# Performance work log

Measured on AMD Instinct MI355X. Metric: run time of the kernel, lower is better.

## Reference

```python
import jax, jax.numpy as jnp
import numpy as np

N_NODES = 50000
N_EDGES = 500000
NEG_SLOPE = 0.2


def gat_conv(h, src, dst, W, attn_l, attn_r, bias, activation):
    """DGL-style GATConv (feat_drop=attn_drop=0, no residual).
    h: [N, F_in]; W: [F_in, H*D]; attn_l/attn_r: [H, D]; bias: [H*D].
    Returns [N, H, D]."""
    H, D = attn_l.shape
    feat = (h @ W).reshape(-1, H, D)                      # [N, H, D]
    el = (feat * attn_l).sum(-1)                          # [N, H]
    er = (feat * attn_r).sum(-1)                          # [N, H]
    e = jax.nn.leaky_relu(el[src] + er[dst], NEG_SLOPE)   # [E, H] edge logits
    # edge softmax over incoming edges of each dst node
    emax = jax.ops.segment_max(e, dst, num_segments=N_NODES)
    emax = jnp.where(jnp.isfinite(emax), emax, 0.0)       # guard zero in-degree
    ee = jnp.exp(e - emax[dst])                           # [E, H]
    denom = jax.ops.segment_sum(ee, dst, num_segments=N_NODES)
    alpha = ee / jnp.maximum(denom[dst], 1e-9)            # [E, H]
    # weighted scatter-aggregate of source features
    out = jax.ops.segment_sum(feat[src] * alpha[..., None], dst,
                              num_segments=N_NODES)       # [N, H, D]
    out = out + bias.reshape(1, H, D)
    return activation(out) if activation is not None else out


def setup_inputs() -> dict:
    key = jax.random.key(0)
    ks = jax.random.split(key, 20)
    in0, in1, hid, heads, ncls = 256, 128, 64, 8, 10

    def xn(k, shape):
        fan = shape[0] + (shape[1] if len(shape) > 1 else shape[0])
        return jax.random.normal(k, shape, jnp.float32) * np.float32(np.sqrt(2.0 / fan)) * 1.414

    inp = {
        "feat0": jax.random.normal(ks[0], (30000, in0), jnp.float32),
        "feat1": jax.random.normal(ks[1], (20000, in1), jnp.float32),
        "fc0_w": xn(ks[2], (in0, hid)), "fc0_b": jnp.zeros((hid,), jnp.float32),
        "fc1_w": xn(ks[3], (in1, hid)), "fc1_b": jnp.zeros((hid,), jnp.float32),
        "W0": xn(ks[4], (hid, heads * hid)),
        "al0": xn(ks[5], (heads, hid)), "ar0": xn(ks[6], (heads, hid)),
        "b0": jnp.zeros((heads * hid,), jnp.float32),
        "W1": xn(ks[7], (heads * hid, heads * hid)),
        "al1": xn(ks[8], (heads, hid)), "ar1": xn(ks[9], (heads, hid)),
        "b1": jnp.zeros((heads * hid,), jnp.float32),
        "W2": xn(ks[10], (heads * hid, 1 * ncls)),
        "al2": xn(ks[11], (1, ncls)), "ar2": xn(ks[12], (1, ncls)),
        "b2": jnp.zeros((ncls,), jnp.float32),
        "edge_index": jax.random.randint(ks[13], (2, N_EDGES), 0, N_NODES, jnp.int64
                                         if jax.config.jax_enable_x64 else jnp.int32),
    }
    return inp


def reference(feat0, feat1, fc0_w, fc0_b, fc1_w, fc1_b,
              W0, al0, ar0, b0, W1, al1, ar1, b1, W2, al2, ar2, b2,
              edge_index):
    src, dst = edge_index[0], edge_index[1]
    # per-type linear projection then concat along node axis
    h = jnp.concatenate([feat0 @ fc0_w + fc0_b, feat1 @ fc1_w + fc1_b], axis=0)
    h = gat_conv(h, src, dst, W0, al0, ar0, b0, jax.nn.elu).reshape(N_NODES, -1)
    h = gat_conv(h, src, dst, W1, al1, ar1, b1, jax.nn.elu).reshape(N_NODES, -1)
    logits = gat_conv(h, src, dst, W2, al2, ar2, b2, None).mean(axis=1)  # [N, ncls]
    return logits
```

## Files before the change

### kernel.cpp

```cpp
#include <hip/hip_runtime.h>
#include <hip/hip_bf16.h>
#include <hip/hip_fp16.h>

#define N_NODES 50000
#define N_EDGES 500000
#define HEADS 8
#define HID 64
#define HD 512
#define NCLS 10
#define M_PAD 50048
#define YTILES_L1 391
#define F0ROWS 30080
#define F1ROWS 20096

typedef _Float16 f16x8 __attribute__((ext_vector_type(8)));
typedef _Float16 h8v   __attribute__((ext_vector_type(8)));
typedef float    f32x4 __attribute__((ext_vector_type(4)));

#define GLD_LDS16(g, l) __builtin_amdgcn_global_load_lds( \
    (__attribute__((address_space(1))) void*)(g),         \
    (__attribute__((address_space(3))) void*)(l), 16, 0, 0)

#define E_N (F0ROWS * 256)
#define F_N (F1ROWS * 128)
#define A_N (512 * 256)
#define B_N (512 * 128)
#define C_N (512 * 512)
#define D_N 1024
#define PREP_TOTAL (E_N + F_N + A_N + B_N + C_N + D_N + N_EDGES)

__global__ void prep(const float* __restrict__ feat0, const float* __restrict__ feat1,
                     const float* __restrict__ fc0_w, const float* __restrict__ fc0_b,
                     const float* __restrict__ fc1_w, const float* __restrict__ fc1_b,
                     const float* __restrict__ W0, const float* __restrict__ W1,
                     const int* __restrict__ dst,
                     _Float16* __restrict__ f0h, _Float16* __restrict__ f1h,
                     _Float16* __restrict__ Wc0t, _Float16* __restrict__ Wc1t,
                     _Float16* __restrict__ W1t, float* __restrict__ biasF,
                     int* __restrict__ cnt) {
    int idx = blockIdx.x * 256 + threadIdx.x;
    if (idx < E_N) {
        int m = idx >> 8, k = idx & 255;
        f0h[idx] = (m < 30000) ? (_Float16)feat0[(size_t)m * 256 + k] : (_Float16)0.f;
        return;
    }
    idx -= E_N;
    if (idx < F_N) {
        int m = idx >> 7, k = idx & 127;
        f1h[idx] = (m < 20000) ? (_Float16)feat1[(size_t)m * 128 + k] : (_Float16)0.f;
        return;
    }
    idx -= F_N;
    if (idx < A_N) {
        int k = idx >> 9, n = idx & 511;
        float s = 0.f;
#pragma unroll 8
        for (int j = 0; j < 64; j++) s += fc0_w[k * 64 + j] * W0[j * 512 + n];
        Wc0t[n * 256 + k] = (_Float16)s;
        return;
    }
    idx -= A_N;
    if (idx < B_N) {
        int k = idx >> 9, n = idx & 511;
        float s = 0.f;
#pragma unroll 8
        for (int j = 0; j < 64; j++) s += fc1_w[k * 64 + j] * W0[j * 512 + n];
        Wc1t[n * 128 + k] = (_Float16)s;
        return;
    }
    idx -= B_N;
    if (idx < C_N) {
        int k = idx >> 9, n = idx & 511;
        W1t[n * 512 + k] = (_Float16)W1[k * 512 + n];
        return;
    }
    idx -= C_N;
    if (idx < D_N) {
        int t = idx >> 9, n = idx & 511;
        const float* fb = t ? fc1_b : fc0_b;
        float s = 0.f;
#pragma unroll 8
        for (int j = 0; j < 64; j++) s += fb[j] * W0[j * 512 + n];
        biasF[t * 512 + n] = s;
        return;
    }
    idx -= D_N;
    if (idx < N_EDGES) atomicAdd(&cnt[dst[idx]], 1);
}

#define NBLK_SCAN 196

__global__ void scan_part(const int* __restrict__ cnt, int* __restrict__ part) {
    __shared__ int s[256];
    int i = blockIdx.x * 256 + threadIdx.x;
    s[threadIdx.x] = (i < N_NODES) ? cnt[i] : 0;
    __syncthreads();
    for (int off = 128; off; off >>= 1) {
        if (threadIdx.x < off) s[threadIdx.x] += s[threadIdx.x + off];
        __syncthreads();
    }
    if (threadIdx.x == 0) part[blockIdx.x] = s[0];
}

__global__ void scan_offs(int* __restrict__ part) {
    __shared__ int s[256];
    int tid = threadIdx.x;
    int v = (tid < NBLK_SCAN) ? part[tid] : 0;
    s[tid] = v;
    __syncthreads();
    for (int off = 1; off < 256; off <<= 1) {
        int x = (tid >= off) ? s[tid - off] : 0;
        __syncthreads();
        s[tid] += x;
        __syncthreads();
    }
    if (tid < NBLK_SCAN) part[tid] = s[tid] - v;
}

__global__ void scan_apply(const int* __restrict__ cnt, const int* __restrict__ part,
                           int* __restrict__ rp, int* __restrict__ cur) {
    __shared__ int s[256];
    int tid = threadIdx.x;
    int i = blockIdx.x * 256 + tid;
    int v = (i < N_NODES) ? cnt[i] : 0;
    s[tid] = v;
    __syncthreads();
    for (int off = 1; off < 256; off <<= 1) {
        int x = (tid >= off) ? s[tid - off] : 0;
        __syncthreads();
        s[tid] += x;
        __syncthreads();
    }
    if (i < N_NODES) {
        int excl = s[tid] - v + part[blockIdx.x];
        rp[i] = excl; cur[i] = excl;
    }
    if (i == 0) rp[N_NODES] = N_EDGES;
}

__device__ __forceinline__ void gemm_tile(
        const _Float16* __restrict__ A, const _Float16* __restrict__ Bt,
        _Float16* __restrict__ Cb, const float* __restrict__ al,
        const float* __restrict__ ar, const float* __restrict__ cbias,
        float* __restrict__ el, float* __restrict__ er,
        int M, int K, int row_off, int ytiles, int bid,
        _Float16* Asl, _Float16* Bsl) {
    int k8 = bid & 7, jj = bid >> 3;
    int y = k8 + 8 * (jj >> 1);
    if (y >= ytiles) return;
    int m0 = y * 128;
    int n0 = (jj & 1) * 256;
    int t = threadIdx.x;
    int lane = t & 63;
    int w = t >> 6;
    int wm = (w & 1) * 64, wn = (w >> 1) * 64;
    int l15 = lane & 15, quad = lane >> 4;
    f32x4 acc[4][4];
#pragma unroll
    for (int i = 0; i < 4; i++)
#pragma unroll
        for (int j = 0; j < 4; j++) acc[i][j] = (f32x4){0.f, 0.f, 0.f, 0.f};

    int fbA = t * 16;
    int rowA = fbA >> 6, kgA = ((fbA >> 4) & 3) ^ (rowA & 3);
    int fbB0 = t * 16;
    int fbB1 = fbB0 + 8192;
    int rowB0 = fbB0 >> 6, kgB0 = ((fbB0 >> 4) & 3) ^ (rowB0 & 3);
    int rowB1 = fbB1 >> 6, kgB1 = ((fbB1 >> 4) & 3) ^ (rowB1 & 3);

    for (int k0 = 0; k0 < K; k0 += 32) {
        GLD_LDS16(A + (size_t)(m0 + rowA) * K + k0 + kgA * 8, (char*)Asl + fbA);
        GLD_LDS16(Bt + (size_t)(n0 + rowB0) * K + k0 + kgB0 * 8, (char*)Bsl + fbB0);
        GLD_LDS16(Bt + (size_t)(n0 + rowB1) * K + k0 + kgB1 * 8, (char*)Bsl + fbB1);
        __syncthreads();
        f16x8 af[4], bfr[4];
#pragma unroll
        for (int i = 0; i < 4; i++) {
            int r = wm + i * 16 + l15;
            int kg = quad ^ (r & 3);
            af[i] = *(const f16x8*)(Asl + r * 32 + kg * 8);
        }
#pragma unroll
        for (int j = 0; j < 4; j++) {
            int r = wn + j * 16 + l15;
            int kg = quad ^ (r & 3);
            bfr[j] = *(const f16x8*)(Bsl + r * 32 + kg * 8);
        }
#pragma unroll
        for (int i = 0; i < 4; i++)
#pragma unroll
            for (int j = 0; j < 4; j++)
                acc[i][j] = __builtin_amdgcn_mfma_f32_16x16x32_f16(af[i], bfr[j], acc[i][j], 0, 0, 0);
        __syncthreads();
    }
    float cb[4];
#pragma unroll
    for (int j = 0; j < 4; j++)
        cb[j] = cbias ? cbias[n0 + wn + j * 16 + l15] : 0.f;
#pragma unroll
    for (int i = 0; i < 4; i++) {
        int rbase = m0 + wm + i * 16 + quad * 4;
#pragma unroll
        for (int j = 0; j < 4; j++) {
            int col = n0 + wn + j * 16 + l15;
#pragma unroll
            for (int r = 0; r < 4; r++) {
                int row = rbase + r;
                if (row < M)
                    Cb[(size_t)(row_off + row) * HD + col] = (_Float16)(acc[i][j][r] + cb[j]);
            }
        }
    }
    int h = (n0 + wn) >> 6;
    float alv[4], arv[4];
#pragma unroll
    for (int j = 0; j < 4; j++) {
        alv[j] = al[h * 64 + j * 16 + l15];
        arv[j] = ar[h * 64 + j * 16 + l15];
    }
#pragma unroll
    for (int i = 0; i < 4; i++) {
#pragma unroll
        for (int r = 0; r < 4; r++) {
            float sl = 0.f, sr = 0.f;
#pragma unroll
            for (int j = 0; j < 4; j++) {
                float v = acc[i][j][r] + cb[j];
                sl += v * alv[j]; sr += v * arv[j];
            }
#pragma unroll
            for (int mk = 1; mk < 16; mk <<= 1) {
                sl += __shfl_xor(sl, mk);
                sr += __shfl_xor(sr, mk);
            }
            int row = m0 + wm + i * 16 + quad * 4 + r;
            if (l15 == 0 && row < M) {
                el[(size_t)(row_off + row) * HEADS + h] = sl;
                er[(size_t)(row_off + row) * HEADS + h] = sr;
            }
        }
    }
}

#define SCAT_BLKS ((N_EDGES + 511) / 512)
#define G0A_BLKS (8 * 2 * ((235 + 7) / 8))
#define G0B_BLKS (8 * 2 * ((157 + 7) / 8))

__global__ __launch_bounds__(512) void scatter_gemm0(
        const int* __restrict__ src, const int* __restrict__ dst,
        int* __restrict__ cursor, int* __restrict__ srcs,
        const _Float16* __restrict__ f0h, const _Float16* __restrict__ Wc0t,
        const _Float16* __restrict__ f1h, const _Float16* __restrict__ Wc1t,
        _Float16* __restrict__ featA, const float* __restrict__ al0,
        const float* __restrict__ ar0, const float* __restrict__ biasF,
        float* __restrict__ el, float* __restrict__ er) {
    __shared__ _Float16 Asl[128 * 32];
    __shared__ _Float16 Bsl[256 * 32];
    int bid = blockIdx.x;
    if (bid < SCAT_BLKS) {
        int t = bid * 512 + threadIdx.x;
        if (t < N_EDGES) {
            int pos = atomicAdd(&cursor[dst[t]], 1);
            srcs[pos] = src[t];
        }
        return;
    }
    bid -= SCAT_BLKS;
    if (bid < G0A_BLKS) {
        gemm_tile(f0h, Wc0t, featA, al0, ar0, biasF, el, er,
                  30000, 256, 0, 235, bid, Asl, Bsl);
        return;
    }
    bid -= G0A_BLKS;
    gemm_tile(f1h, Wc1t, featA, al0, ar0, biasF + 512, el, er,
              20000, 128, 30000, 157, bid, Asl, Bsl);
}

__global__ __launch_bounds__(512) void gemm_mfma_wide(const _Float16* __restrict__ A,
                                                      const _Float16* __restrict__ Bt,
                                                      _Float16* __restrict__ Cb,
                                                      const float* __restrict__ al,
                                                      const float* __restrict__ ar,
                                                      float* __restrict__ el,
                                                      float* __restrict__ er,
                                                      int M, int K, int ytiles) {
    __shared__ _Float16 Asl[128 * 32];
    __shared__ _Float16 Bsl[256 * 32];
    gemm_tile(A, Bt, Cb, al, ar, nullptr, el, er, M, K, 0, ytiles,
              blockIdx.x, Asl, Bsl);
}

__global__ __launch_bounds__(64) void attn_agg(
        const int* __restrict__ rp, const int* __restrict__ srcs,
        const float* __restrict__ el, const float* __restrict__ er,
        const _Float16* __restrict__ feat, const float* __restrict__ bias,
        _Float16* __restrict__ out) {
    __shared__ float aS[592];
    __shared__ int   sS[64];
    int lane = threadIdx.x;
    int n    = blockIdx.x;
    int s0 = rp[n], s1 = rp[n + 1];
    int deg = s1 - s0;
    float er8[8];
    {
        f32x4 a = *(const f32x4*)(er + (size_t)n * 8);
        f32x4 b = *(const f32x4*)(er + (size_t)n * 8 + 4);
        er8[0]=a[0]; er8[1]=a[1]; er8[2]=a[2]; er8[3]=a[3];
        er8[4]=b[0]; er8[5]=b[1]; er8[6]=b[2]; er8[7]=b[3];
    }
    bool fast = (deg <= 64);
    if (fast) {
        bool act = lane < deg;
        int sp = act ? srcs[s0 + lane] : 0;
        sS[lane] = sp;
        f32x4 ea = {0.f,0.f,0.f,0.f}, eb = {0.f,0.f,0.f,0.f};
        if (act) {
            ea = *(const f32x4*)(el + (size_t)sp * 8);
            eb = *(const f32x4*)(el + (size_t)sp * 8 + 4);
        }
        float e8[8] = {ea[0],ea[1],ea[2],ea[3],eb[0],eb[1],eb[2],eb[3]};
#pragma unroll
        for (int h = 0; h < 8; h++) {
            float e = e8[h] + er8[h];
            e = e > 0.f ? e : 0.2f * e;
            e8[h] = act ? e : -1e30f;
        }
#pragma unroll
        for (int h = 0; h < 8; h++) {
            float mm = e8[h];
#pragma unroll
            for (int mk = 1; mk < 64; mk <<= 1) mm = fmaxf(mm, __shfl_xor(mm, mk));
            float pv = act ? __expf(e8[h] - mm) : 0.f;
            float ss = pv;
#pragma unroll
            for (int mk = 1; mk < 64; mk <<= 1) ss += __shfl_xor(ss, mk);
            aS[lane * 9 + h] = pv * (1.f / fmaxf(ss, 1e-9f));
        }
    } else {
        float m8[8], s8[8];
#pragma unroll
        for (int h = 0; h < 8; h++) { m8[h] = -1e30f; s8[h] = 0.f; }
        for (int base = s0; base < s1; base += 64) {
            bool act = base + lane < s1;
            int sp = act ? srcs[base + lane] : 0;
            f32x4 ea = {0.f,0.f,0.f,0.f}, eb = {0.f,0.f,0.f,0.f};
            if (act) {
                ea = *(const f32x4*)(el + (size_t)sp * 8);
                eb = *(const f32x4*)(el + (size_t)sp * 8 + 4);
            }
            float ev[8] = {ea[0],ea[1],ea[2],ea[3],eb[0],eb[1],eb[2],eb[3]};
#pragma unroll
            for (int h = 0; h < 8; h++) {
                float e = ev[h] + er8[h];
                e = e > 0.f ? e : 0.2f * e;
                e = act ? e : -1e30f;
                float cm = e;
#pragma unroll
                for (int mk = 1; mk < 64; mk <<= 1) cm = fmaxf(cm, __shfl_xor(cm, mk));
                float nm = fmaxf(m8[h], cm);
                float pv = act ? __expf(e - nm) : 0.f;
#pragma unroll
                for (int mk = 1; mk < 64; mk <<= 1) pv += __shfl_xor(pv, mk);
                s8[h] = s8[h] * __expf(m8[h] - nm) + pv;
                m8[h] = nm;
            }
        }
        if (lane == 0) {
#pragma unroll
            for (int h = 0; h < 8; h++) {
                aS[576 + h] = 1.f / fmaxf(s8[h], 1e-9f);
                aS[584 + h] = m8[h];
            }
        }
    }
    __builtin_amdgcn_wave_barrier();
    int hh = lane >> 3, d0 = (lane & 7) * 8;
    h8v z = {(_Float16)0, (_Float16)0, (_Float16)0, (_Float16)0,
             (_Float16)0, (_Float16)0, (_Float16)0, (_Float16)0};
    h8v acc0 = z, acc1 = z, acc2 = z, acc3 = z;
    const _Float16* colbase = feat + hh * 64 + d0;
    if (fast) {
        int p = 0;
        for (; p + 4 <= deg; p += 4) {
            int spa = sS[p],     spb = sS[p + 1];
            int spc = sS[p + 2], spd = sS[p + 3];
            _Float16 aa = (_Float16)aS[p * 9 + hh];
            _Float16 ab = (_Float16)aS[(p + 1) * 9 + hh];
            _Float16 ac = (_Float16)aS[(p + 2) * 9 + hh];
            _Float16 ad = (_Float16)aS[(p + 3) * 9 + hh];
            h8v fa = *(const h8v*)(colbase + (size_t)spa * HD);
            h8v fb = *(const h8v*)(colbase + (size_t)spb * HD);
            h8v fc = *(const h8v*)(colbase + (size_t)spc * HD);
            h8v fd = *(const h8v*)(colbase + (size_t)spd * HD);
            h8v a8a = {aa, aa, aa, aa, aa, aa, aa, aa};
            h8v a8b = {ab, ab, ab, ab, ab, ab, ab, ab};
            h8v a8c = {ac, ac, ac, ac, ac, ac, ac, ac};
            h8v a8d = {ad, ad, ad, ad, ad, ad, ad, ad};
            acc0 += a8a * fa;
            acc1 += a8b * fb;
            acc2 += a8c * fc;
            acc3 += a8d * fd;
        }
        for (; p < deg; p++) {
            int sp = sS[p];
            _Float16 ah = (_Float16)aS[p * 9 + hh];
            h8v a8 = {ah, ah, ah, ah, ah, ah, ah, ah};
            h8v f = *(const h8v*)(colbase + (size_t)sp * HD);
            acc0 += a8 * f;
        }
    } else {
        float inv_l = aS[576 + hh];
        float m_l   = aS[584 + hh];
        float ern_l = er[(size_t)n * 8 + hh];
        for (int p = s0; p < s1; p++) {
            int sp = srcs[p];
            float e = el[(size_t)sp * 8 + hh] + ern_l;
            e = e > 0.f ? e : 0.2f * e;
            _Float16 ah = (_Float16)(__expf(e - m_l) * inv_l);
            h8v a8 = {ah, ah, ah, ah, ah, ah, ah, ah};
            h8v f = *(const h8v*)(colbase + (size_t)sp * HD);
            acc0 += a8 * f;
        }
    }
    acc0 += acc1; acc2 += acc3; acc0 += acc2;
    float4 b0v = *(const float4*)(bias + lane * 8);
    float4 b1v = *(const float4*)(bias + lane * 8 + 4);
    float bb[8] = {b0v.x,b0v.y,b0v.z,b0v.w,b1v.x,b1v.y,b1v.z,b1v.w};
    h8v o;
#pragma unroll
    for (int j = 0; j < 8; j++) {
        float x = (float)acc0[j] + bb[j];
        x = x > 0.f ? x : __expf(x) - 1.f;
        o[j] = (_Float16)x;
    }
    *(h8v*)(out + (size_t)n * HD + lane * 8) = o;
}

__global__ __launch_bounds__(256) void gemm_n10v2(
        const _Float16* __restrict__ A, const float* __restrict__ B,
        const float* __restrict__ al2, const float* __restrict__ ar2,
        float* __restrict__ C, float* __restrict__ el, float* __restrict__ er) {
    __shared__ float Bs[512 * 11];
    int t = threadIdx.x;
    for (int i = t; i < 512 * NCLS; i += 256) {
        int k = i / NCLS, c = i - k * NCLS;
        Bs[k * 11 + c] = B[i];
    }
    __syncthreads();
    int lane = t & 63;
    int m = blockIdx.x * 4 + (t >> 6);
    float acc[NCLS];
#pragma unroll
    for (int c = 0; c < NCLS; c++) acc[c] = 0.f;
    const _Float16* a = A + (size_t)m * HD;
#pragma unroll
    for (int j = 0; j < 8; j++) {
        float av = (float)a[j * 64 + lane];
        const float* br = Bs + (j * 64 + lane) * 11;
#pragma unroll
        for (int c = 0; c < NCLS; c++) acc[c] += av * br[c];
    }
#pragma unroll
    for (int c = 0; c < NCLS; c++)
#pragma unroll
        for (int mk = 1; mk < 64; mk <<= 1) acc[c] += __shfl_xor(acc[c], mk);
    if (lane == 0) {
        float e1 = 0.f, e2 = 0.f;
#pragma unroll
        for (int c = 0; c < NCLS; c++) { e1 += acc[c] * al2[c]; e2 += acc[c] * ar2[c]; }
        el[m] = e1; er[m] = e2;
#pragma unroll
        for (int c = 0; c < NCLS; c++) C[(size_t)m * NCLS + c] = acc[c];
    }
}

__global__ __launch_bounds__(64) void attn2_agg2(
        const int* __restrict__ rp, const int* __restrict__ srcs,
        const float* __restrict__ el, const float* __restrict__ er,
        const float* __restrict__ feat2, const float* __restrict__ b2,
        float* __restrict__ out) {
    int lane = threadIdx.x;
    int n = blockIdx.x;
    int s0 = rp[n], s1 = rp[n + 1], deg = s1 - s0;
    float ern = er[n];
    float facc[NCLS];
#pragma unroll
    for (int c = 0; c < NCLS; c++) facc[c] = 0.f;
    if (deg <= 64) {
        bool act = lane < deg;
        int sp = act ? srcs[s0 + lane] : 0;
        float e = act ? el[sp] + ern : 0.f;
        e = e > 0.f ? e : 0.2f * e;
        if (!act) e = -1e30f;
        float mm = e;
#pragma unroll
        for (int mk = 1; mk < 64; mk <<= 1) mm = fmaxf(mm, __shfl_xor(mm, mk));
        float pv = act ? __expf(e - mm) : 0.f;
        float ss = pv;
#pragma unroll
        for (int mk = 1; mk < 64; mk <<= 1) ss += __shfl_xor(ss, mk);
        float a = pv / fmaxf(ss, 1e-9f);
        if (act) {
#pragma unroll
            for (int c = 0; c < NCLS; c++) facc[c] = a * feat2[(size_t)sp * NCLS + c];
        }
    } else {
        float mm = -1e30f, ssum = 0.f;
        for (int base = s0; base < s1; base += 64) {
            bool act = base + lane < s1;
            int sp = act ? srcs[base + lane] : 0;
            float e = act ? el[sp] + ern : 0.f;
            e = e > 0.f ? e : 0.2f * e;
            if (!act) e = -1e30f;
            float cm = e;
#pragma unroll
            for (int mk = 1; mk < 64; mk <<= 1) cm = fmaxf(cm, __shfl_xor(cm, mk));
            float nm = fmaxf(mm, cm);
            float pv = act ? __expf(e - nm) : 0.f;
#pragma unroll
            for (int mk = 1; mk < 64; mk <<= 1) pv += __shfl_xor(pv, mk);
            ssum = ssum * __expf(mm - nm) + pv;
            mm = nm;
        }
        float inv = 1.f / fmaxf(ssum, 1e-9f);
        for (int base = s0; base < s1; base += 64) {
            bool act = base + lane < s1;
            int sp = act ? srcs[base + lane] : 0;
            float e = act ? el[sp] + ern : 0.f;
            e = e > 0.f ? e : 0.2f * e;
            float a = act ? __expf(e - mm) * inv : 0.f;
            if (act) {
#pragma unroll
                for (int c = 0; c < NCLS; c++) facc[c] += a * feat2[(size_t)sp * NCLS + c];
            }
        }
    }
#pragma unroll
    for (int c = 0; c < NCLS; c++)
#pragma unroll
        for (int mk = 1; mk < 64; mk <<= 1) facc[c] += __shfl_xor(facc[c], mk);
    if (lane == 0) {
#pragma unroll
        for (int c = 0; c < NCLS; c++) out[(size_t)n * NCLS + c] = facc[c] + b2[c];
    }
}

extern "C" void kernel_launch(void* const* d_in, const int* in_sizes, int n_in,
                              void* d_out, int out_size, void* d_ws, size_t ws_size,
                              hipStream_t stream) {
    const float* feat0 = (const float*)d_in[0];
    const float* feat1 = (const float*)d_in[1];
    const float* fc0_w = (const float*)d_in[2];
    const float* fc0_b = (const float*)d_in[3];
    const float* fc1_w = (const float*)d_in[4];
    const float* fc1_b = (const float*)d_in[5];
    const float* W0    = (const float*)d_in[6];
    const float* al0   = (const float*)d_in[7];
    const float* ar0   = (const float*)d_in[8];
    const float* b0    = (const float*)d_in[9];
    const float* W1    = (const float*)d_in[10];
    const float* al1   = (const float*)d_in[11];
    const float* ar1   = (const float*)d_in[12];
    const float* b1    = (const float*)d_in[13];
    const float* W2    = (const float*)d_in[14];
    const float* al2   = (const float*)d_in[15];
    const float* ar2   = (const float*)d_in[16];
    const float* b2    = (const float*)d_in[17];
    const int* eidx    = (const int*)d_in[18];
    const int* src = eidx;
    const int* dst = eidx + N_EDGES;
    float* out = (float*)d_out;

    char* ws = (char*)d_ws;
    size_t off = 0;
    auto alloc = [&](size_t bytes) { size_t o = off; off = (off + bytes + 255) & ~(size_t)255; return o; };

    _Float16* featA = (_Float16*)(ws + alloc((size_t)M_PAD * HD * 2));
    _Float16* aggh  = (_Float16*)(ws + alloc((size_t)M_PAD * HD * 2));
    _Float16* f0h   = (_Float16*)(ws + alloc((size_t)F0ROWS * 256 * 2));
    _Float16* f1h   = (_Float16*)(ws + alloc((size_t)F1ROWS * 128 * 2));
    float*    feat2 = (float*)(ws + alloc((size_t)N_NODES * NCLS * 4));
    float*    el    = (float*)(ws + alloc((size_t)N_NODES * HEADS * 4));
    float*    er    = (float*)(ws + alloc((size_t)N_NODES * HEADS * 4));
    float*    el2   = (float*)(ws + alloc((size_t)N_NODES * 4));
    float*    er2   = (float*)(ws + alloc((size_t)N_NODES * 4));
    float*    biasF = (float*)(ws + alloc(1024 * 4));
    int*      cnt   = (int*)  (ws + alloc((size_t)N_NODES * 4));
    int*      rp    = (int*)  (ws + alloc((size_t)(N_NODES + 1) * 4));
    int*      cur   = (int*)  (ws + alloc((size_t)N_NODES * 4));
    int*      srcs  = (int*)  (ws + alloc((size_t)N_EDGES * 4));
    int*      part  = (int*)  (ws + alloc(1024));
    _Float16* Wc0t  = (_Float16*)(ws + alloc(512 * 256 * 2));
    _Float16* Wc1t  = (_Float16*)(ws + alloc(512 * 128 * 2));
    _Float16* W1t   = (_Float16*)(ws + alloc(512 * 512 * 2));

    hipMemsetAsync(cnt, 0, N_NODES * sizeof(int), stream);
    prep<<<(PREP_TOTAL + 255) / 256, 256, 0, stream>>>(
        feat0, feat1, fc0_w, fc0_b, fc1_w, fc1_b, W0, W1, dst,
        f0h, f1h, Wc0t, Wc1t, W1t, biasF, cnt);

    scan_part<<<NBLK_SCAN, 256, 0, stream>>>(cnt, part);
    scan_offs<<<1, 256, 0, stream>>>(part);
    scan_apply<<<NBLK_SCAN, 256, 0, stream>>>(cnt, part, rp, cur);

    scatter_gemm0<<<SCAT_BLKS + G0A_BLKS + G0B_BLKS, 512, 0, stream>>>(
        src, dst, cur, srcs, f0h, Wc0t, f1h, Wc1t, featA, al0, ar0, biasF, el, er);

    attn_agg<<<N_NODES, 64, 0, stream>>>(rp, srcs, el, er, featA, b0, aggh);

    int g1 = 8 * 2 * ((YTILES_L1 + 7) / 8);
    gemm_mfma_wide<<<g1, 512, 0, stream>>>(aggh, W1t, featA, al1, ar1, el, er,
                                           N_NODES, HD, YTILES_L1);
    attn_agg<<<N_NODES, 64, 0, stream>>>(rp, srcs, el, er, featA, b1, aggh);

    gemm_n10v2<<<N_NODES / 4, 256, 0, stream>>>(aggh, W2, al2, ar2, feat2, el2, er2);
    attn2_agg2<<<N_NODES, 64, 0, stream>>>(rp, srcs, el2, er2, feat2, b2, out);
}
```

Measured before the change: 529.5 us.

## Pack four destination nodes per wave in attention aggregation kernel

Reworks the attention-aggregate kernel so each 64-lane wave handles four destination nodes with 16 lanes each, rather than one node per wave. Each lane now covers 32 output columns across four head pairs, and the softmax reductions use 16-lane shuffles. The aim is to cut wasted lanes and per-block overhead, since average in-degree is about 10 and most lanes sat idle before. In exchange, nodes with degree above 16 take the slower online-softmax path, and the four nodes in a wave can diverge on degree.

```diff
diff --git a/kernel.cpp b/kernel.cpp
--- a/kernel.cpp
+++ b/kernel.cpp
@@ -290,15 +290,18 @@
               blockIdx.x, Asl, Bsl);
 }
 
-__global__ __launch_bounds__(64) void attn_agg(
+__global__ __launch_bounds__(64) void attn_agg4(
         const int* __restrict__ rp, const int* __restrict__ srcs,
         const float* __restrict__ el, const float* __restrict__ er,
         const _Float16* __restrict__ feat, const float* __restrict__ bias,
         _Float16* __restrict__ out) {
-    __shared__ float aS[592];
+    __shared__ float aS[576];
     __shared__ int   sS[64];
     int lane = threadIdx.x;
-    int n    = blockIdx.x;
+    int g    = lane >> 4;
+    int gl   = lane & 15;
+    int hi   = gl >> 3;
+    int n    = blockIdx.x * 4 + g;
     int s0 = rp[n], s1 = rp[n + 1];
     int deg = s1 - s0;
     float er8[8];
@@ -308,10 +311,11 @@
         er8[0]=a[0]; er8[1]=a[1]; er8[2]=a[2]; er8[3]=a[3];
         er8[4]=b[0]; er8[5]=b[1]; er8[6]=b[2]; er8[7]=b[3];
     }
-    bool fast = (deg <= 64);
+    bool fast = (deg <= 16);
+    float m8[8], s8[8];
     if (fast) {
-        bool act = lane < deg;
-        int sp = act ? srcs[s0 + lane] : 0;
+        bool act = gl < deg;
+        int sp = act ? srcs[s0 + gl] : 0;
         sS[lane] = sp;
         f32x4 ea = {0.f,0.f,0.f,0.f}, eb = {0.f,0.f,0.f,0.f};
         if (act) {
@@ -329,20 +333,19 @@
         for (int h = 0; h < 8; h++) {
             float mm = e8[h];
 #pragma unroll
-            for (int mk = 1; mk < 64; mk <<= 1) mm = fmaxf(mm, __shfl_xor(mm, mk));
+            for (int mk = 1; mk < 16; mk <<= 1) mm = fmaxf(mm, __shfl_xor(mm, mk));
             float pv = act ? __expf(e8[h] - mm) : 0.f;
             float ss = pv;
 #pragma unroll
-            for (int mk = 1; mk < 64; mk <<= 1) ss += __shfl_xor(ss, mk);
-            aS[lane * 9 + h] = pv * (1.f / fmaxf(ss, 1e-9f));
+            for (int mk = 1; mk < 16; mk <<= 1) ss += __shfl_xor(ss, mk);
+            aS[g * 144 + gl * 9 + h] = pv * (1.f / fmaxf(ss, 1e-9f));
         }
     } else {
-        float m8[8], s8[8];
 #pragma unroll
         for (int h = 0; h < 8; h++) { m8[h] = -1e30f; s8[h] = 0.f; }
-        for (int base = s0; base < s1; base += 64) {
-            bool act = base + lane < s1;
-            int sp = act ? srcs[base + lane] : 0;
+        for (int base = s0; base < s1; base += 16) {
+            bool act = base + gl < s1;
+            int sp = act ? srcs[base + gl] : 0;
             f32x4 ea = {0.f,0.f,0.f,0.f}, eb = {0.f,0.f,0.f,0.f};
             if (act) {
                 ea = *(const f32x4*)(el + (size_t)sp * 8);
@@ -356,84 +359,97 @@
                 e = act ? e : -1e30f;
                 float cm = e;
 #pragma unroll
-                for (int mk = 1; mk < 64; mk <<= 1) cm = fmaxf(cm, __shfl_xor(cm, mk));
+                for (int mk = 1; mk < 16; mk <<= 1) cm = fmaxf(cm, __shfl_xor(cm, mk));
                 float nm = fmaxf(m8[h], cm);
                 float pv = act ? __expf(e - nm) : 0.f;
 #pragma unroll
-                for (int mk = 1; mk < 64; mk <<= 1) pv += __shfl_xor(pv, mk);
+                for (int mk = 1; mk < 16; mk <<= 1) pv += __shfl_xor(pv, mk);
                 s8[h] = s8[h] * __expf(m8[h] - nm) + pv;
                 m8[h] = nm;
             }
         }
-        if (lane == 0) {
-#pragma unroll
-            for (int h = 0; h < 8; h++) {
-                aS[576 + h] = 1.f / fmaxf(s8[h], 1e-9f);
-                aS[584 + h] = m8[h];
-            }
-        }
+#pragma unroll
+        for (int h = 0; h < 8; h++) s8[h] = 1.f / fmaxf(s8[h], 1e-9f);
     }
     __builtin_amdgcn_wave_barrier();
-    int hh = lane >> 3, d0 = (lane & 7) * 8;
     h8v z = {(_Float16)0, (_Float16)0, (_Float16)0, (_Float16)0,
              (_Float16)0, (_Float16)0, (_Float16)0, (_Float16)0};
-    h8v acc0 = z, acc1 = z, acc2 = z, acc3 = z;
-    const _Float16* colbase = feat + hh * 64 + d0;
+    h8v accA[4] = {z, z, z, z};
+    h8v accB[4] = {z, z, z, z};
+    const _Float16* fb = feat + gl * 8;
     if (fast) {
         int p = 0;
-        for (; p + 4 <= deg; p += 4) {
-            int spa = sS[p],     spb = sS[p + 1];
-            int spc = sS[p + 2], spd = sS[p + 3];
-            _Float16 aa = (_Float16)aS[p * 9 + hh];
-            _Float16 ab = (_Float16)aS[(p + 1) * 9 + hh];
-            _Float16 ac = (_Float16)aS[(p + 2) * 9 + hh];
-            _Float16 ad = (_Float16)aS[(p + 3) * 9 + hh];
-            h8v fa = *(const h8v*)(colbase + (size_t)spa * HD);
-            h8v fb = *(const h8v*)(colbase + (size_t)spb * HD);
-            h8v fc = *(const h8v*)(colbase + (size_t)spc * HD);
-            h8v fd = *(const h8v*)(colbase + (size_t)spd * HD);
-            h8v a8a = {aa, aa, aa, aa, aa, aa, aa, aa};
-            h8v a8b = {ab, ab, ab, ab, ab, ab, ab, ab};
-            h8v a8c = {ac, ac, ac, ac, ac, ac, ac, ac};
-            h8v a8d = {ad, ad, ad, ad, ad, ad, ad, ad};
-            acc0 += a8a * fa;
-            acc1 += a8b * fb;
-            acc2 += a8c * fc;
-            acc3 += a8d * fd;
-        }
-        for (; p < deg; p++) {
-            int sp = sS[p];
-            _Float16 ah = (_Float16)aS[p * 9 + hh];
-            h8v a8 = {ah, ah, ah, ah, ah, ah, ah, ah};
-            h8v f = *(const h8v*)(colbase + (size_t)sp * HD);
-            acc0 += a8 * f;
+        for (; p + 2 <= deg; p += 2) {
+            int spa = sS[g * 16 + p];
+            int spb = sS[g * 16 + p + 1];
+            h8v fA[4], fB[4];
+#pragma unroll
+            for (int q = 0; q < 4; q++)
+                fA[q] = *(const h8v*)(fb + (size_t)spa * HD + q * 128);
+#pragma unroll
+            for (int q = 0; q < 4; q++)
+                fB[q] = *(const h8v*)(fb + (size_t)spb * HD + q * 128);
+#pragma unroll
+            for (int q = 0; q < 4; q++) {
+                _Float16 ha = (_Float16)aS[g * 144 + p * 9 + q * 2 + hi];
+                h8v va = {ha, ha, ha, ha, ha, ha, ha, ha};
+                accA[q] += va * fA[q];
+            }
+#pragma unroll
+            for (int q = 0; q < 4; q++) {
+                _Float16 hb = (_Float16)aS[g * 144 + (p + 1) * 9 + q * 2 + hi];
+                h8v vb = {hb, hb, hb, hb, hb, hb, hb, hb};
+                accB[q] += vb * fB[q];
+            }
+        }
+        if (p < deg) {
+            int sp = sS[g * 16 + p];
+            h8v fA[4];
+#pragma unroll
+            for (int q = 0; q < 4; q++)
+                fA[q] = *(const h8v*)(fb + (size_t)sp * HD + q * 128);
+#pragma unroll
+            for (int q = 0; q < 4; q++) {
+                _Float16 ha = (_Float16)aS[g * 144 + p * 9 + q * 2 + hi];
+                h8v va = {ha, ha, ha, ha, ha, ha, ha, ha};
+                accA[q] += va * fA[q];
+            }
         }
     } else {
-        float inv_l = aS[576 + hh];
-        float m_l   = aS[584 + hh];
-        float ern_l = er[(size_t)n * 8 + hh];
         for (int p = s0; p < s1; p++) {
             int sp = srcs[p];
-            float e = el[(size_t)sp * 8 + hh] + ern_l;
-            e = e > 0.f ? e : 0.2f * e;
-            _Float16 ah = (_Float16)(__expf(e - m_l) * inv_l);
-            h8v a8 = {ah, ah, ah, ah, ah, ah, ah, ah};
-            h8v f = *(const h8v*)(colbase + (size_t)sp * HD);
-            acc0 += a8 * f;
-        }
-    }
-    acc0 += acc1; acc2 += acc3; acc0 += acc2;
-    float4 b0v = *(const float4*)(bias + lane * 8);
-    float4 b1v = *(const float4*)(bias + lane * 8 + 4);
-    float bb[8] = {b0v.x,b0v.y,b0v.z,b0v.w,b1v.x,b1v.y,b1v.z,b1v.w};
-    h8v o;
-#pragma unroll
-    for (int j = 0; j < 8; j++) {
-        float x = (float)acc0[j] + bb[j];
-        x = x > 0.f ? x : __expf(x) - 1.f;
-        o[j] = (_Float16)x;
-    }
-    *(h8v*)(out + (size_t)n * HD + lane * 8) = o;
+            h8v fA[4];
+#pragma unroll
+            for (int q = 0; q < 4; q++)
+                fA[q] = *(const h8v*)(fb + (size_t)sp * HD + q * 128);
+#pragma unroll
+            for (int q = 0; q < 4; q++) {
+                int h = q * 2 + hi;
+                float e = el[(size_t)sp * 8 + h] + er8[h];
+                e = e > 0.f ? e : 0.2f * e;
+                _Float16 ha = (_Float16)(__expf(e - m8[h]) * s8[h]);
+                h8v va = {ha, ha, ha, ha, ha, ha, ha, ha};
+                accA[q] += va * fA[q];
+            }
+        }
+    }
+#pragma unroll
+    for (int q = 0; q < 4; q++) accA[q] += accB[q];
+#pragma unroll
+    for (int q = 0; q < 4; q++) {
+        int col = q * 128 + gl * 8;
+        float4 b0v = *(const float4*)(bias + col);
+        float4 b1v = *(const float4*)(bias + col + 4);
+        float bb[8] = {b0v.x,b0v.y,b0v.z,b0v.w,b1v.x,b1v.y,b1v.z,b1v.w};
+        h8v o;
+#pragma unroll
+        for (int j = 0; j < 8; j++) {
+            float x = (float)accA[q][j] + bb[j];
+            x = x > 0.f ? x : __expf(x) - 1.f;
+            o[j] = (_Float16)x;
+        }
+        *(h8v*)(out + (size_t)n * HD + col) = o;
+    }
 }
 
 __global__ __launch_bounds__(256) void gemm_n10v2(
@@ -606,12 +622,12 @@
     scatter_gemm0<<<SCAT_BLKS + G0A_BLKS + G0B_BLKS, 512, 0, stream>>>(
         src, dst, cur, srcs, f0h, Wc0t, f1h, Wc1t, featA, al0, ar0, biasF, el, er);
 
-    attn_agg<<<N_NODES, 64, 0, stream>>>(rp, srcs, el, er, featA, b0, aggh);
+    attn_agg4<<<N_NODES / 4, 64, 0, stream>>>(rp, srcs, el, er, featA, b0, aggh);
 
     int g1 = 8 * 2 * ((YTILES_L1 + 7) / 8);
     gemm_mfma_wide<<<g1, 512, 0, stream>>>(aggh, W1t, featA, al1, ar1, el, er,
                                            N_NODES, HD, YTILES_L1);
-    attn_agg<<<N_NODES, 64, 0, stream>>>(rp, srcs, el, er, featA, b1, aggh);
+    attn_agg4<<<N_NODES / 4, 64, 0, stream>>>(rp, srcs, el, er, featA, b1, aggh);
 
     gemm_n10v2<<<N_NODES / 4, 256, 0, stream>>>(aggh, W2, al2, ar2, feat2, el2, er2);
     attn2_agg2<<<N_NODES, 64, 0, stream>>>(rp, srcs, el2, er2, feat2, b2, out);
```

After: 548.9 us. 1.04x slower.
